# Kernel optimization log

Measured on AMD Instinct MI355X. Metric: run time of the kernel, lower is better.

Reference implementation:

```python
import jax, jax.numpy as jnp
import numpy as np

N_ATOMS = 8192
N_PAIRS = 65536
F = 128        # n_atombasis
R = 20         # n_radialbasis
B = 5          # graph_n_blocks
EPS = 1e-8     # stability constant


def setup_inputs() -> dict:
    key = jax.random.key(0)
    ks = jax.random.split(key, 16)
    rn = lambda k, shape, s=0.05: jax.random.normal(k, shape, dtype=jnp.float32) * s
    return {
        "features": jax.random.normal(ks[0], (N_ATOMS, F), jnp.float32),
        "distances": jax.random.uniform(ks[1], (N_PAIRS,), jnp.float32, 0.5, 5.0),
        "vectors": jax.random.normal(ks[2], (N_PAIRS, 3), jnp.float32),
        "cutoffs": jax.random.uniform(ks[3], (N_PAIRS,), jnp.float32),
        "rbfs": jax.random.normal(ks[4], (N_PAIRS, R), jnp.float32),
        "filter_W": rn(ks[5], (R, B * 3 * F)),
        "filter_b": jnp.zeros((B * 3 * F,), jnp.float32),
        "int_W1": rn(ks[6], (B, F, F)),
        "int_b1": jnp.zeros((B, F), jnp.float32),
        "int_W2": rn(ks[7], (B, F, 3 * F)),
        "int_b2": jnp.zeros((B, 3 * F), jnp.float32),
        "mix_Wv": rn(ks[8], (B, F, 2 * F)),
        "mix_W1": rn(ks[9], (B, 2 * F, F)),
        "mix_b1": jnp.zeros((B, F), jnp.float32),
        "mix_W2": rn(ks[10], (B, F, 3 * F)),
        "mix_b2": jnp.zeros((B, 3 * F), jnp.float32),
        "idx_i": jax.random.randint(ks[11], (N_PAIRS,), 0, N_ATOMS),
        "idx_j": jax.random.randint(ks[12], (N_PAIRS,), 0, N_ATOMS),
    }


def reference(features, distances, vectors, cutoffs, rbfs,
              filter_W, filter_b, int_W1, int_b1, int_W2, int_b2,
              mix_Wv, mix_W1, mix_b1, mix_W2, mix_b2, idx_i, idx_j):
    n_atoms = features.shape[0]
    # Cutoff-weighted radial filters, one (3F) chunk per block: [P, B*3F]
    descriptors = (rbfs @ filter_W + filter_b) * cutoffs[:, None]
    dir_ij = vectors / distances[:, None]                       # [P, 3]

    q = features[:, None, :]                                    # [N, 1, F]
    mu = jnp.zeros((n_atoms, 3, F), dtype=features.dtype)       # [N, 3, F]

    for b in range(B):
        # --- interaction block ---
        x = jax.nn.silu(q @ int_W1[b] + int_b1[b]) @ int_W2[b] + int_b2[b]  # [N,1,3F]
        Wij = descriptors[:, None, b * 3 * F:(b + 1) * 3 * F]               # [P,1,3F]
        xj = x[idx_j] * Wij                                                 # [P,1,3F]
        muj = mu[idx_j]                                                     # [P,3,F]
        dq, dmuR, dmumu = jnp.split(xj, 3, axis=-1)                         # [P,1,F] each
        dmu = dmuR * dir_ij[:, :, None] + dmumu * muj                       # [P,3,F]
        q = q + jax.ops.segment_sum(dq, idx_i, num_segments=n_atoms)
        mu = mu + jax.ops.segment_sum(dmu, idx_i, num_segments=n_atoms)

        # --- mixing block ---
        mu_V, mu_W = jnp.split(mu @ mix_Wv[b], 2, axis=-1)                  # [N,3,F] each
        mu_Vn = jnp.sqrt(jnp.sum(mu_V ** 2, axis=-2, keepdims=True) + EPS)  # [N,1,F]
        ctx = jnp.concatenate([q, mu_Vn], axis=-1)                          # [N,1,2F]
        y = jax.nn.silu(ctx @ mix_W1[b] + mix_b1[b]) @ mix_W2[b] + mix_b2[b]
        dq_i, dmu_i, dqmu_i = jnp.split(y, 3, axis=-1)                      # [N,1,F] each
        q = q + dq_i + dqmu_i * jnp.sum(mu_V * mu_W, axis=1, keepdims=True)
        mu = mu + dmu_i * mu_W

    return q[:, 0, :], mu
```

## Files before the change

### kernel.cpp

```cpp
#include <hip/hip_runtime.h>
#include <hip/hip_bf16.h>

#define NA 8192
#define NP 65536
#define WROW 1920
#define CAP 40

typedef short short8 __attribute__((ext_vector_type(8)));
typedef short short4v __attribute__((ext_vector_type(4)));
typedef float floatx4 __attribute__((ext_vector_type(4)));

static __device__ __forceinline__ short f2bf(float f) {
    union { float f; unsigned u; } v; v.f = f;
    unsigned r = v.u + 0x7FFF + ((v.u >> 16) & 1);
    return (short)(r >> 16);
}
static __device__ __forceinline__ float bf2f(short s) {
    union { unsigned u; float f; } v;
    v.u = ((unsigned)(unsigned short)s) << 16;
    return v.f;
}
static __device__ __forceinline__ unsigned char f2fp8(float f) {
    int p = __builtin_amdgcn_cvt_pk_fp8_f32(f, 0.f, 0, false);
    return (unsigned char)(p & 0xFF);
}
static __device__ __forceinline__ float fp82f(unsigned char b) {
    return __builtin_amdgcn_cvt_f32_fp8((int)b, 0);
}
static __device__ __forceinline__ float silu(float v) {
    return v / (1.f + __expf(-v));
}

static __device__ __forceinline__ void swz(const float* __restrict__ src,
                                           short* __restrict__ dst,
                                           int K, int N, int idx) {
    int kn = K * N;
    int b = idx / kn;
    int r = idx - b * kn;
    int tile = r >> 9, li = r & 511;
    int lane = li >> 3, bb = li & 7;
    int Kt = K >> 5;
    int nt = tile / Kt, kt = tile - nt * Kt;
    int k = kt * 32 + (lane >> 4) * 8 + bb;
    int n = nt * 16 + (lane & 15);
    dst[idx] = f2bf(src[b * kn + k * N + n]);
}

__global__ __launch_bounds__(256) void k_setup(const float* __restrict__ iW1,
                                               const float* __restrict__ iW2,
                                               const float* __restrict__ mWv,
                                               const float* __restrict__ mW1,
                                               const float* __restrict__ mW2,
                                               const float* __restrict__ fW,
                                               short* __restrict__ W1t,
                                               short* __restrict__ W2t,
                                               short* __restrict__ Wvt,
                                               short* __restrict__ mW1t,
                                               short* __restrict__ mW2t,
                                               short* __restrict__ fWt,
                                               const float* __restrict__ feat,
                                               float* __restrict__ q,
                                               float* __restrict__ mu,
                                               short* __restrict__ q_bf,
                                               unsigned* __restrict__ xarr0,
                                               unsigned* __restrict__ muarr0,
                                               int* __restrict__ cursor) {
    int idx = blockIdx.x * 256 + threadIdx.x;
    if (idx < 962560) {
        if (idx < 81920)       { swz(iW1, W1t, 128, 128, idx); return; }
        idx -= 81920;
        if (idx < 245760)      { swz(iW2, W2t, 128, 384, idx); return; }
        idx -= 245760;
        if (idx < 163840)      { swz(mWv, Wvt, 128, 256, idx); return; }
        idx -= 163840;
        if (idx < 163840)      { swz(mW1, mW1t, 256, 128, idx); return; }
        idx -= 163840;
        if (idx < 245760)      { swz(mW2, mW2t, 128, 384, idx); return; }
        idx -= 245760;
        {
            int b = idx / 12288;
            int r = idx - b * 12288;
            int nt = r >> 9;
            int li = r & 511;
            int lane = li >> 3, bb = li & 7;
            int k = (lane >> 4) * 8 + bb;
            int n = nt * 16 + (lane & 15);
            fWt[b * 12288 + r] = (k < 20) ? f2bf(fW[k * WROW + b * 384 + n]) : (short)0;
        }
        return;
    }
    idx -= 962560;
    if (idx < NA * 128) { float v = feat[idx]; q[idx] = v; q_bf[idx] = f2bf(v); xarr0[idx] = 0u; }
    if (idx < NA * 256) muarr0[idx] = 0u;
    mu[idx] = 0.f;
    if (idx < NA) cursor[idx] = 0;
}

__global__ __launch_bounds__(256) void k_fillprep(const int* __restrict__ idx_i,
                                                  const int* __restrict__ idx_j,
                                                  int* __restrict__ cursor,
                                                  const float* __restrict__ cut,
                                                  const float* __restrict__ dist,
                                                  const float* __restrict__ vec,
                                                  const float* __restrict__ rbfs,
                                                  float* __restrict__ cut_csr,
                                                  float4* __restrict__ dirj,
                                                  short* __restrict__ rbf_c) {
    int p = blockIdx.x * 256 + threadIdx.x;
    if (p >= NP) return;
    int i = idx_i[p];
    int pos = atomicAdd(&cursor[i], 1);
    if (pos >= CAP) return;
    int e = i * CAP + pos;
    float c = cut[p];
    cut_csr[e] = c;
    float invd = 1.f / dist[p];
    float4 d;
    d.x = vec[p * 3 + 0] * invd;
    d.y = vec[p * 3 + 1] * invd;
    d.z = vec[p * 3 + 2] * invd;
    d.w = __int_as_float(idx_j[p]);
    dirj[e] = d;
    #pragma unroll
    for (int k = 0; k < 20; ++k) rbf_c[e * 32 + k] = f2bf(rbfs[p * 20 + k] * c);
    #pragma unroll
    for (int k = 20; k < 32; ++k) rbf_c[e * 32 + k] = 0;
}

__global__ __launch_bounds__(256) void k_x(const short* __restrict__ q_bf,
                                           const short* __restrict__ W1sw,
                                           const short* __restrict__ W2sw,
                                           const float* __restrict__ b1,
                                           const float* __restrict__ b2,
                                           unsigned char* __restrict__ xarr) {
    __shared__ __align__(16) short qtile[16 * 136];
    __shared__ __align__(16) short hs[16 * 136];
    int t = threadIdx.x;
    int wv = t >> 6, lane = t & 63, quad = lane >> 4, l16 = lane & 15;
    int a0 = blockIdx.x * 16;

    #pragma unroll
    for (int it = 0; it < 2; ++it) {
        int c = it * 256 + t;
        int row = c >> 5, col4 = c & 31;
        *(short4v*)(qtile + row * 136 + col4 * 4) =
            *(const short4v*)(q_bf + (a0 + row) * 128 + col4 * 4);
    }
    __syncthreads();

    floatx4 acc0 = {0.f, 0.f, 0.f, 0.f}, acc1 = {0.f, 0.f, 0.f, 0.f};
    #pragma unroll
    for (int kk = 0; kk < 4; ++kk) {
        short8 a  = *(const short8*)(qtile + l16 * 136 + kk * 32 + quad * 8);
        short8 b0 = *(const short8*)(W1sw + ((wv * 2 + 0) * 4 + kk) * 512 + lane * 8);
        short8 bq = *(const short8*)(W1sw + ((wv * 2 + 1) * 4 + kk) * 512 + lane * 8);
        acc0 = __builtin_amdgcn_mfma_f32_16x16x32_bf16(a, b0, acc0, 0, 0, 0);
        acc1 = __builtin_amdgcn_mfma_f32_16x16x32_bf16(a, bq, acc1, 0, 0, 0);
    }
    __syncthreads();
    {
        int n0 = wv * 32 + l16;
        float bia0 = b1[n0], bia1 = b1[n0 + 16];
        #pragma unroll
        for (int r = 0; r < 4; ++r) {
            int m = quad * 4 + r;
            hs[m * 136 + n0]      = f2bf(silu(acc0[r] + bia0));
            hs[m * 136 + n0 + 16] = f2bf(silu(acc1[r] + bia1));
        }
    }
    __syncthreads();
    floatx4 acc[6];
    #pragma unroll
    for (int jj = 0; jj < 6; ++jj) acc[jj] = {0.f, 0.f, 0.f, 0.f};
    #pragma unroll
    for (int kk = 0; kk < 4; ++kk) {
        short8 a = *(const short8*)(hs + l16 * 136 + kk * 32 + quad * 8);
        #pragma unroll
        for (int jj = 0; jj < 6; ++jj) {
            short8 b = *(const short8*)(W2sw + ((wv * 6 + jj) * 4 + kk) * 512 + lane * 8);
            acc[jj] = __builtin_amdgcn_mfma_f32_16x16x32_bf16(a, b, acc[jj], 0, 0, 0);
        }
    }
    #pragma unroll
    for (int jj = 0; jj < 6; ++jj) {
        int n = wv * 96 + jj * 16 + l16;
        float bia = b2[n];
        #pragma unroll
        for (int r = 0; r < 4; ++r) {
            int m = quad * 4 + r;
            xarr[(size_t)((a0 + m) * 128 + (n & 127)) * 4 + (n >> 7)] =
                f2fp8(acc[jj][r] + bia);
        }
    }
}

__global__ __launch_bounds__(256, 4) void k_gather(const unsigned* __restrict__ xarr_r,
                                                   const uint2* __restrict__ muarr_r,
                                                   const short* __restrict__ rbf_c,
                                                   const short* __restrict__ fWt,
                                                   const float* __restrict__ fbp,
                                                   const float4* __restrict__ dirj,
                                                   const float* __restrict__ cut_csr,
                                                   const int* __restrict__ cursor,
                                                   short* __restrict__ dqg,
                                                   short* __restrict__ dmug) {
    __shared__ short dlds[16 * 392];
    __shared__ float pm[3 * 512];
    int i = blockIdx.x;
    int t = threadIdx.x;
    int wv = t >> 6, lane = t & 63, quad = lane >> 4, l16 = lane & 15;
    int start = i * CAP;

    float4 dj[4];
    #pragma unroll
    for (int m = 0; m < 4; ++m) dj[m] = dirj[start + wv + 4 * m];
    short8 afrag = *(const short8*)(rbf_c + (size_t)(start + l16) * 32 + quad * 8);
    float cc[4];
    #pragma unroll
    for (int r = 0; r < 4; ++r) cc[r] = cut_csr[start + quad * 4 + r];

    int cnt = cursor[i];
    if (cnt > CAP) cnt = CAP;
    int end = start + cnt;

    float acc[8];
    #pragma unroll
    for (int k = 0; k < 8; ++k) acc[k] = 0.f;

    for (int e0 = start; e0 < end; e0 += 16) {
        if (e0 > start) {
            __syncthreads();
            #pragma unroll
            for (int m = 0; m < 4; ++m) dj[m] = dirj[e0 + wv + 4 * m];
            afrag = *(const short8*)(rbf_c + (size_t)(e0 + l16) * 32 + quad * 8);
            #pragma unroll
            for (int r = 0; r < 4; ++r) cc[r] = cut_csr[e0 + quad * 4 + r];
        }
        int clen = end - e0; if (clen > 16) clen = 16;
        #pragma unroll
        for (int nt = 0; nt < 6; ++nt) {
            int col = wv * 96 + nt * 16 + l16;
            short8 bfr = *(const short8*)(fWt + (wv * 6 + nt) * 512 + lane * 8);
            floatx4 z = {0.f, 0.f, 0.f, 0.f};
            floatx4 ad = __builtin_amdgcn_mfma_f32_16x16x32_bf16(afrag, bfr, z, 0, 0, 0);
            float fbv = fbp[col];
            dlds[(quad * 4 + 0) * 392 + col] = f2bf(ad[0] + fbv * cc[0]);
            dlds[(quad * 4 + 1) * 392 + col] = f2bf(ad[1] + fbv * cc[1]);
            dlds[(quad * 4 + 2) * 392 + col] = f2bf(ad[2] + fbv * cc[2]);
            dlds[(quad * 4 + 3) * 392 + col] = f2bf(ad[3] + fbv * cc[3]);
        }
        unsigned xl[4], xh[4]; uint2 ml[4], mh[4];
        #pragma unroll
        for (int m = 0; m < 4; ++m) {
            int le = wv + 4 * m;
            int j = (le < clen) ? __float_as_int(dj[m].w) : 0;
            const unsigned* xb_ = xarr_r + (size_t)j * 128 + lane;
            xl[m] = xb_[0];
            xh[m] = xb_[64];
            const uint2* mb_ = muarr_r + (size_t)j * 128 + lane;
            ml[m] = mb_[0];
            mh[m] = mb_[64];
        }
        __syncthreads();
        #pragma unroll
        for (int m = 0; m < 4; ++m) {
            int le = wv + 4 * m;
            if (le < clen) {
                float wa0 = bf2f(dlds[le * 392 + lane]);
                float wb0 = bf2f(dlds[le * 392 + 128 + lane]);
                float wc0 = bf2f(dlds[le * 392 + 256 + lane]);
                float wa1 = bf2f(dlds[le * 392 + 64 + lane]);
                float wb1 = bf2f(dlds[le * 392 + 192 + lane]);
                float wc1 = bf2f(dlds[le * 392 + 320 + lane]);
                {
                    float x0 = fp82f((unsigned char)(xl[m] & 0xFF));
                    float x1 = fp82f((unsigned char)((xl[m] >> 8) & 0xFF));
                    float x2 = fp82f((unsigned char)((xl[m] >> 16) & 0xFF));
                    float u0 = bf2f((short)(ml[m].x & 0xFFFF));
                    float u1 = bf2f((short)(ml[m].x >> 16));
                    float u2 = bf2f((short)(ml[m].y & 0xFFFF));
                    acc[0] += x0 * wa0;
                    float xb = x1 * wb0, xc = x2 * wc0;
                    acc[1] += xb * dj[m].x + xc * u0;
                    acc[2] += xb * dj[m].y + xc * u1;
                    acc[3] += xb * dj[m].z + xc * u2;
                }
                {
                    float x0 = fp82f((unsigned char)(xh[m] & 0xFF));
                    float x1 = fp82f((unsigned char)((xh[m] >> 8) & 0xFF));
                    float x2 = fp82f((unsigned char)((xh[m] >> 16) & 0xFF));
                    float u0 = bf2f((short)(mh[m].x & 0xFFFF));
                    float u1 = bf2f((short)(mh[m].x >> 16));
                    float u2 = bf2f((short)(mh[m].y & 0xFFFF));
                    acc[4] += x0 * wa1;
                    float xb = x1 * wb1, xc = x2 * wc1;
                    acc[5] += xb * dj[m].x + xc * u0;
                    acc[6] += xb * dj[m].y + xc * u1;
                    acc[7] += xb * dj[m].z + xc * u2;
                }
            }
        }
    }
    if (wv) {
        float* p = pm + (wv - 1) * 512;
        #pragma unroll
        for (int arr = 0; arr < 4; ++arr) {
            p[arr * 128 + lane]      = acc[arr];
            p[arr * 128 + 64 + lane] = acc[arr + 4];
        }
    }
    __syncthreads();
    if (wv == 0) {
        #pragma unroll
        for (int hi = 0; hi < 2; ++hi) {
            int f = lane + hi * 64;
            float s[4];
            #pragma unroll
            for (int arr = 0; arr < 4; ++arr)
                s[arr] = acc[arr + 4 * hi]
                       + pm[0 * 512 + arr * 128 + f]
                       + pm[1 * 512 + arr * 128 + f]
                       + pm[2 * 512 + arr * 128 + f];
            dqg[i * 128 + f]            = f2bf(s[0]);
            dmug[(i * 3 + 0) * 128 + f] = f2bf(s[1]);
            dmug[(i * 3 + 1) * 128 + f] = f2bf(s[2]);
            dmug[(i * 3 + 2) * 128 + f] = f2bf(s[3]);
        }
    }
}

__global__ __launch_bounds__(512, 4) void k_mixx(const float* __restrict__ mu_ro,
                                                 const short* __restrict__ dmug,
                                                 const float* __restrict__ q_ro,
                                                 const short* __restrict__ dqg,
                                                 const short* __restrict__ Wvsw,
                                                 const short* __restrict__ W1sw,
                                                 const short* __restrict__ W2sw,
                                                 const float* __restrict__ b1,
                                                 const float* __restrict__ b2,
                                                 float* __restrict__ q,
                                                 float* __restrict__ mu,
                                                 unsigned* __restrict__ xarr_w,
                                                 uint2* __restrict__ muarr_w,
                                                 const short* __restrict__ xW1sw,
                                                 const short* __restrict__ xW2sw,
                                                 const float* __restrict__ xb1,
                                                 const float* __restrict__ xb2,
                                                 int do_x) {
    __shared__ __align__(16) char smem[51968];
    short* ms    = (short*)(smem);
    short* qtile = (short*)(smem + 13056);
    short* Vv    = (short*)(smem + 17408);
    short* hs    = (short*)(smem + 17408);
    short* Vw    = (short*)(smem + 30464);
    short* vnb   = (short*)(smem + 43520);
    short* sb    = (short*)(smem + 47872);
    unsigned char* xls = (unsigned char*)(smem + 43520);
    int t = threadIdx.x;
    int wv = t >> 6, lane = t & 63, quad = lane >> 4, l16 = lane & 15;
    int a0 = blockIdx.x * 16;
    int co = wv * 16 + l16;

    float qnf[4];
    float mnf[4][3];
    #pragma unroll
    for (int r = 0; r < 4; ++r) {
        int m = quad * 4 + r;
        int ga = a0 + m;
        int gq = ga * 128 + co;
        qnf[r] = q_ro[gq] + bf2f(dqg[gq]);
        qtile[m * 136 + co] = f2bf(qnf[r]);
        #pragma unroll
        for (int d = 0; d < 3; ++d) {
            int gm = (ga * 3 + d) * 128 + co;
            mnf[r][d] = mu_ro[gm] + bf2f(dmug[gm]);
            ms[(m * 3 + d) * 136 + co] = f2bf(mnf[r][d]);
        }
    }
    __syncthreads();

    {
        floatx4 acc[3][2];
        #pragma unroll
        for (int mt = 0; mt < 3; ++mt)
            #pragma unroll
            for (int nt = 0; nt < 2; ++nt) acc[mt][nt] = {0.f, 0.f, 0.f, 0.f};
        #pragma unroll
        for (int kk = 0; kk < 4; ++kk) {
            short8 a[3];
            #pragma unroll
            for (int mt = 0; mt < 3; ++mt)
                a[mt] = *(const short8*)(ms + (mt * 16 + l16) * 136 + kk * 32 + quad * 8);
            #pragma unroll
            for (int nt = 0; nt < 2; ++nt) {
                short8 b = *(const short8*)(Wvsw + ((wv * 2 + nt) * 4 + kk) * 512 + lane * 8);
                #pragma unroll
                for (int mt = 0; mt < 3; ++mt)
                    acc[mt][nt] = __builtin_amdgcn_mfma_f32_16x16x32_bf16(a[mt], b, acc[mt][nt], 0, 0, 0);
            }
        }
        #pragma unroll
        for (int mt = 0; mt < 3; ++mt)
            #pragma unroll
            for (int nt = 0; nt < 2; ++nt)
                #pragma unroll
                for (int r = 0; r < 4; ++r) {
                    int row = mt * 16 + quad * 4 + r;
                    int col = wv * 32 + nt * 16 + l16;
                    short v = f2bf(acc[mt][nt][r]);
                    if (col < 128) Vv[row * 136 + col] = v;
                    else           Vw[row * 136 + col - 128] = v;
                }
    }
    __syncthreads();
    #pragma unroll
    for (int k = 0; k < 4; ++k) {
        int idx = k * 512 + t;
        int a = idx >> 7, c = idx & 127;
        float v0 = bf2f(Vv[(a * 3 + 0) * 136 + c]);
        float v1 = bf2f(Vv[(a * 3 + 1) * 136 + c]);
        float v2 = bf2f(Vv[(a * 3 + 2) * 136 + c]);
        float w0 = bf2f(Vw[(a * 3 + 0) * 136 + c]);
        float w1 = bf2f(Vw[(a * 3 + 1) * 136 + c]);
        float w2 = bf2f(Vw[(a * 3 + 2) * 136 + c]);
        vnb[a * 136 + c] = f2bf(sqrtf(v0 * v0 + v1 * v1 + v2 * v2 + 1e-8f));
        sb[a * 128 + c]  = f2bf(v0 * w0 + v1 * w1 + v2 * w2);
    }
    __syncthreads();
    {
        floatx4 acc0 = {0.f, 0.f, 0.f, 0.f};
        #pragma unroll
        for (int kk = 0; kk < 8; ++kk) {
            short8 a;
            if (kk < 4)
                a = *(const short8*)(qtile + l16 * 136 + kk * 32 + quad * 8);
            else
                a = *(const short8*)(vnb + l16 * 136 + (kk - 4) * 32 + quad * 8);
            short8 b0 = *(const short8*)(W1sw + (wv * 8 + kk) * 512 + lane * 8);
            acc0 = __builtin_amdgcn_mfma_f32_16x16x32_bf16(a, b0, acc0, 0, 0, 0);
        }
        int n0 = wv * 16 + l16;
        float bia0 = b1[n0];
        #pragma unroll
        for (int r = 0; r < 4; ++r) {
            int m = quad * 4 + r;
            hs[m * 136 + n0] = f2bf(silu(acc0[r] + bia0));
        }
    }
    __syncthreads();
    {
        floatx4 accB[3];
        #pragma unroll
        for (int c = 0; c < 3; ++c) accB[c] = {0.f, 0.f, 0.f, 0.f};
        #pragma unroll
        for (int kk = 0; kk < 4; ++kk) {
            short8 a = *(const short8*)(hs + l16 * 136 + kk * 32 + quad * 8);
            #pragma unroll
            for (int c = 0; c < 3; ++c) {
                short8 b = *(const short8*)(W2sw + ((c * 8 + wv) * 4 + kk) * 512 + lane * 8);
                accB[c] = __builtin_amdgcn_mfma_f32_16x16x32_bf16(a, b, accB[c], 0, 0, 0);
            }
        }
        float bq_  = b2[co];
        float bm_  = b2[128 + co];
        float bqm_ = b2[256 + co];
        #pragma unroll
        for (int r = 0; r < 4; ++r) {
            int m = quad * 4 + r;
            int ga = a0 + m;
            float dq   = accB[0][r] + bq_;
            float dmu  = accB[1][r] + bm_;
            float dqmu = accB[2][r] + bqm_;
            float sv = bf2f(sb[m * 128 + co]);
            int gq = ga * 128 + co;
            float qn = qnf[r] + dq + dqmu * sv;
            q[gq] = qn;
            qtile[m * 136 + co] = f2bf(qn);
            float mn[3];
            #pragma unroll
            for (int d = 0; d < 3; ++d) {
                int gm = (ga * 3 + d) * 128 + co;
                float mw = bf2f(Vw[(m * 3 + d) * 136 + co]);
                mn[d] = mnf[r][d] + dmu * mw;
                mu[gm] = mn[d];
            }
            if (do_x) {
                uint2 mw2;
                mw2.x = (unsigned)(unsigned short)f2bf(mn[0]) |
                        ((unsigned)(unsigned short)f2bf(mn[1]) << 16);
                mw2.y = (unsigned)(unsigned short)f2bf(mn[2]);
                muarr_w[gq] = mw2;
            }
        }
    }
    if (!do_x) return;
    __syncthreads();
    {
        floatx4 acc0 = {0.f, 0.f, 0.f, 0.f};
        #pragma unroll
        for (int kk = 0; kk < 4; ++kk) {
            short8 a  = *(const short8*)(qtile + l16 * 136 + kk * 32 + quad * 8);
            short8 b0 = *(const short8*)(xW1sw + (wv * 4 + kk) * 512 + lane * 8);
            acc0 = __builtin_amdgcn_mfma_f32_16x16x32_bf16(a, b0, acc0, 0, 0, 0);
        }
        int n0 = wv * 16 + l16;
        float bia0 = xb1[n0];
        #pragma unroll
        for (int r = 0; r < 4; ++r) {
            int m = quad * 4 + r;
            hs[m * 136 + n0] = f2bf(silu(acc0[r] + bia0));
        }
    }
    __syncthreads();
    {
        floatx4 acc[3];
        #pragma unroll
        for (int jj = 0; jj < 3; ++jj) acc[jj] = {0.f, 0.f, 0.f, 0.f};
        #pragma unroll
        for (int kk = 0; kk < 4; ++kk) {
            short8 a = *(const short8*)(hs + l16 * 136 + kk * 32 + quad * 8);
            #pragma unroll
            for (int jj = 0; jj < 3; ++jj) {
                short8 b = *(const short8*)(xW2sw + ((wv * 3 + jj) * 4 + kk) * 512 + lane * 8);
                acc[jj] = __builtin_amdgcn_mfma_f32_16x16x32_bf16(a, b, acc[jj], 0, 0, 0);
            }
        }
        #pragma unroll
        for (int jj = 0; jj < 3; ++jj) {
            int n = wv * 48 + jj * 16 + l16;
            float bia = xb2[n];
            #pragma unroll
            for (int r = 0; r < 4; ++r) {
                int m = quad * 4 + r;
                xls[(m * 128 + (n & 127)) * 4 + (n >> 7)] = f2fp8(acc[jj][r] + bia);
            }
        }
    }
    __syncthreads();
    {
        const unsigned* xlsu = (const unsigned*)xls;
        unsigned* xw = xarr_w + (size_t)a0 * 128;
        #pragma unroll
        for (int k = 0; k < 4; ++k) {
            int idx = k * 512 + t;
            xw[idx] = xlsu[idx];
        }
    }
}

extern "C" void kernel_launch(void* const* d_in, const int* in_sizes, int n_in,
                              void* d_out, int out_size, void* d_ws, size_t ws_size,
                              hipStream_t stream) {
    const float* feat = (const float*)d_in[0];
    const float* dist = (const float*)d_in[1];
    const float* vec  = (const float*)d_in[2];
    const float* cut  = (const float*)d_in[3];
    const float* rbfs = (const float*)d_in[4];
    const float* fW   = (const float*)d_in[5];
    const float* fb   = (const float*)d_in[6];
    const float* iW1  = (const float*)d_in[7];
    const float* ib1  = (const float*)d_in[8];
    const float* iW2  = (const float*)d_in[9];
    const float* ib2  = (const float*)d_in[10];
    const float* mWv  = (const float*)d_in[11];
    const float* mW1  = (const float*)d_in[12];
    const float* mb1  = (const float*)d_in[13];
    const float* mW2  = (const float*)d_in[14];
    const float* mb2  = (const float*)d_in[15];
    const int* idx_i  = (const int*)d_in[16];
    const int* idx_j  = (const int*)d_in[17];

    float* q  = (float*)d_out;
    float* mu = (float*)d_out + NA * 128;

    char* w = (char*)d_ws;
    unsigned* xarr0  = (unsigned*)(w);
    unsigned* xarr1  = (unsigned*)(w + 4194304);
    uint2*    muarr0 = (uint2*)(w + 8388608);
    uint2*    muarr1 = (uint2*)(w + 16777216);
    short* dqg     = (short*)(w + 25165824);
    short* dmug    = (short*)(w + 27262976);
    short* q_bf    = (short*)(w + 33554432);
    short* W1t     = (short*)(w + 35651584);
    short* W2t     = (short*)(w + 35815424);
    short* Wvt     = (short*)(w + 36306944);
    short* mW1t    = (short*)(w + 36634624);
    short* mW2t    = (short*)(w + 36962304);
    short* fWt     = (short*)(w + 37453824);
    int*   cursor  = (int*)(w + 37576704);
    float4* dirj   = (float4*)(w + 37609472);
    float* cut_csr = (float*)(w + 42852608);
    short* rbf_c   = (short*)(w + 44163392);

    k_setup<<<16048, 256, 0, stream>>>(iW1, iW2, mWv, mW1, mW2, fW,
                                       W1t, W2t, Wvt, mW1t, mW2t, fWt,
                                       feat, q, mu, q_bf, xarr0, (unsigned*)muarr0, cursor);
    k_fillprep<<<NP / 256, 256, 0, stream>>>(idx_i, idx_j, cursor, cut, dist, vec,
                                             rbfs, cut_csr, dirj, rbf_c);

    k_x<<<NA / 16, 256, 0, stream>>>(q_bf, W1t, W2t, ib1, ib2, (unsigned char*)xarr0);
    unsigned* xa[2] = {xarr0, xarr1};
    uint2*    ma[2] = {muarr0, muarr1};
    for (int b = 0; b < 5; ++b) {
        int bn = (b + 1) % 5;
        k_gather<<<NA, 256, 0, stream>>>(xa[b & 1], ma[b & 1], rbf_c, fWt + b * 12288,
                                         fb + b * 384, dirj, cut_csr, cursor,
                                         dqg, dmug);
        k_mixx<<<NA / 16, 512, 0, stream>>>(mu, dmug, q, dqg,
                                            Wvt + b * 32768,
                                            mW1t + b * 32768, mW2t + b * 49152,
                                            mb1 + b * 128, mb2 + b * 384,
                                            q, mu,
                                            xa[(b + 1) & 1], ma[(b + 1) & 1],
                                            W1t + bn * 16384, W2t + bn * 49152,
                                            ib1 + bn * 128, ib2 + bn * 384,
                                            (b < 4) ? 1 : 0);
    }
}
```

Measured before the change: 368.9 us.

## Vectorize gather loads, split mixing MFMA chains, use memsets for zero-init

The gather kernel now has each lane own two adjacent features, so x, mu, descriptor and partial-sum accesses become wider vector loads and stores in place of pairs of strided scalar ones. The mixing MLP's first layer splits its single 8-step MFMA dependency chain into two independent 4-step chains that are summed afterwards, which exposes more instruction-level parallelism. Zero-initialisation of cursor, mu and muarr0 moves from the setup kernel to hipMemsetAsync calls, and xarr0 is no longer zeroed. This shrinks the setup grid but adds three extra stream operations and changes the lane-to-feature mapping.

```diff
diff --git a/kernel.cpp b/kernel.cpp
--- a/kernel.cpp
+++ b/kernel.cpp
@@ -60,11 +60,7 @@
                                                short* __restrict__ fWt,
                                                const float* __restrict__ feat,
                                                float* __restrict__ q,
-                                               float* __restrict__ mu,
-                                               short* __restrict__ q_bf,
-                                               unsigned* __restrict__ xarr0,
-                                               unsigned* __restrict__ muarr0,
-                                               int* __restrict__ cursor) {
+                                               short* __restrict__ q_bf) {
     int idx = blockIdx.x * 256 + threadIdx.x;
     if (idx < 962560) {
         if (idx < 81920)       { swz(iW1, W1t, 128, 128, idx); return; }
@@ -90,10 +86,7 @@
         return;
     }
     idx -= 962560;
-    if (idx < NA * 128) { float v = feat[idx]; q[idx] = v; q_bf[idx] = f2bf(v); xarr0[idx] = 0u; }
-    if (idx < NA * 256) muarr0[idx] = 0u;
-    mu[idx] = 0.f;
-    if (idx < NA) cursor[idx] = 0;
+    if (idx < NA * 128) { float v = feat[idx]; q[idx] = v; q_bf[idx] = f2bf(v); }
 }
 
 __global__ __launch_bounds__(256) void k_fillprep(const int* __restrict__ idx_i,
@@ -210,6 +203,7 @@
     int t = threadIdx.x;
     int wv = t >> 6, lane = t & 63, quad = lane >> 4, l16 = lane & 15;
     int start = i * CAP;
+    int f0 = lane * 2;
 
     float4 dj[4];
     #pragma unroll
@@ -249,36 +243,33 @@
             dlds[(quad * 4 + 2) * 392 + col] = f2bf(ad[2] + fbv * cc[2]);
             dlds[(quad * 4 + 3) * 392 + col] = f2bf(ad[3] + fbv * cc[3]);
         }
-        unsigned xl[4], xh[4]; uint2 ml[4], mh[4];
+        uint2 xr[4]; uint4 mr[4];
         #pragma unroll
         for (int m = 0; m < 4; ++m) {
             int le = wv + 4 * m;
             int j = (le < clen) ? __float_as_int(dj[m].w) : 0;
-            const unsigned* xb_ = xarr_r + (size_t)j * 128 + lane;
-            xl[m] = xb_[0];
-            xh[m] = xb_[64];
-            const uint2* mb_ = muarr_r + (size_t)j * 128 + lane;
-            ml[m] = mb_[0];
-            mh[m] = mb_[64];
+            xr[m] = *(const uint2*)(xarr_r + (size_t)j * 128 + f0);
+            mr[m] = *(const uint4*)(muarr_r + (size_t)j * 128 + f0);
         }
         __syncthreads();
         #pragma unroll
         for (int m = 0; m < 4; ++m) {
             int le = wv + 4 * m;
             if (le < clen) {
-                float wa0 = bf2f(dlds[le * 392 + lane]);
-                float wb0 = bf2f(dlds[le * 392 + 128 + lane]);
-                float wc0 = bf2f(dlds[le * 392 + 256 + lane]);
-                float wa1 = bf2f(dlds[le * 392 + 64 + lane]);
-                float wb1 = bf2f(dlds[le * 392 + 192 + lane]);
-                float wc1 = bf2f(dlds[le * 392 + 320 + lane]);
+                unsigned wa = *(const unsigned*)(dlds + le * 392 + f0);
+                unsigned wb = *(const unsigned*)(dlds + le * 392 + 128 + f0);
+                unsigned wc = *(const unsigned*)(dlds + le * 392 + 256 + f0);
+                float wa0 = bf2f((short)(wa & 0xFFFF)), wa1 = bf2f((short)(wa >> 16));
+                float wb0 = bf2f((short)(wb & 0xFFFF)), wb1 = bf2f((short)(wb >> 16));
+                float wc0 = bf2f((short)(wc & 0xFFFF)), wc1 = bf2f((short)(wc >> 16));
                 {
-                    float x0 = fp82f((unsigned char)(xl[m] & 0xFF));
-                    float x1 = fp82f((unsigned char)((xl[m] >> 8) & 0xFF));
-                    float x2 = fp82f((unsigned char)((xl[m] >> 16) & 0xFF));
-                    float u0 = bf2f((short)(ml[m].x & 0xFFFF));
-                    float u1 = bf2f((short)(ml[m].x >> 16));
-                    float u2 = bf2f((short)(ml[m].y & 0xFFFF));
+                    unsigned xw = xr[m].x;
+                    float x0 = fp82f((unsigned char)(xw & 0xFF));
+                    float x1 = fp82f((unsigned char)((xw >> 8) & 0xFF));
+                    float x2 = fp82f((unsigned char)((xw >> 16) & 0xFF));
+                    float u0 = bf2f((short)(mr[m].x & 0xFFFF));
+                    float u1 = bf2f((short)(mr[m].x >> 16));
+                    float u2 = bf2f((short)(mr[m].y & 0xFFFF));
                     acc[0] += x0 * wa0;
                     float xb = x1 * wb0, xc = x2 * wc0;
                     acc[1] += xb * dj[m].x + xc * u0;
@@ -286,12 +277,13 @@
                     acc[3] += xb * dj[m].z + xc * u2;
                 }
                 {
-                    float x0 = fp82f((unsigned char)(xh[m] & 0xFF));
-                    float x1 = fp82f((unsigned char)((xh[m] >> 8) & 0xFF));
-                    float x2 = fp82f((unsigned char)((xh[m] >> 16) & 0xFF));
-                    float u0 = bf2f((short)(mh[m].x & 0xFFFF));
-                    float u1 = bf2f((short)(mh[m].x >> 16));
-                    float u2 = bf2f((short)(mh[m].y & 0xFFFF));
+                    unsigned xw = xr[m].y;
+                    float x0 = fp82f((unsigned char)(xw & 0xFF));
+                    float x1 = fp82f((unsigned char)((xw >> 8) & 0xFF));
+                    float x2 = fp82f((unsigned char)((xw >> 16) & 0xFF));
+                    float u0 = bf2f((short)(mr[m].z & 0xFFFF));
+                    float u1 = bf2f((short)(mr[m].z >> 16));
+                    float u2 = bf2f((short)(mr[m].w & 0xFFFF));
                     acc[4] += x0 * wa1;
                     float xb = x1 * wb1, xc = x2 * wc1;
                     acc[5] += xb * dj[m].x + xc * u0;
@@ -305,26 +297,23 @@
         float* p = pm + (wv - 1) * 512;
         #pragma unroll
         for (int arr = 0; arr < 4; ++arr) {
-            p[arr * 128 + lane]      = acc[arr];
-            p[arr * 128 + 64 + lane] = acc[arr + 4];
+            float2 v; v.x = acc[arr]; v.y = acc[arr + 4];
+            *(float2*)(p + arr * 128 + f0) = v;
         }
     }
     __syncthreads();
     if (wv == 0) {
         #pragma unroll
-        for (int hi = 0; hi < 2; ++hi) {
-            int f = lane + hi * 64;
-            float s[4];
-            #pragma unroll
-            for (int arr = 0; arr < 4; ++arr)
-                s[arr] = acc[arr + 4 * hi]
-                       + pm[0 * 512 + arr * 128 + f]
-                       + pm[1 * 512 + arr * 128 + f]
-                       + pm[2 * 512 + arr * 128 + f];
-            dqg[i * 128 + f]            = f2bf(s[0]);
-            dmug[(i * 3 + 0) * 128 + f] = f2bf(s[1]);
-            dmug[(i * 3 + 1) * 128 + f] = f2bf(s[2]);
-            dmug[(i * 3 + 2) * 128 + f] = f2bf(s[3]);
+        for (int arr = 0; arr < 4; ++arr) {
+            float2 p0 = *(const float2*)(pm + 0 * 512 + arr * 128 + f0);
+            float2 p1 = *(const float2*)(pm + 1 * 512 + arr * 128 + f0);
+            float2 p2 = *(const float2*)(pm + 2 * 512 + arr * 128 + f0);
+            float sl = acc[arr]     + p0.x + p1.x + p2.x;
+            float sh = acc[arr + 4] + p0.y + p1.y + p2.y;
+            unsigned o = (unsigned)(unsigned short)f2bf(sl) |
+                         ((unsigned)(unsigned short)f2bf(sh) << 16);
+            if (arr == 0) *(unsigned*)(dqg + i * 128 + f0) = o;
+            else          *(unsigned*)(dmug + (i * 3 + arr - 1) * 128 + f0) = o;
         }
     }
 }
@@ -428,23 +417,23 @@
     }
     __syncthreads();
     {
-        floatx4 acc0 = {0.f, 0.f, 0.f, 0.f};
-        #pragma unroll
-        for (int kk = 0; kk < 8; ++kk) {
-            short8 a;
-            if (kk < 4)
-                a = *(const short8*)(qtile + l16 * 136 + kk * 32 + quad * 8);
-            else
-                a = *(const short8*)(vnb + l16 * 136 + (kk - 4) * 32 + quad * 8);
-            short8 b0 = *(const short8*)(W1sw + (wv * 8 + kk) * 512 + lane * 8);
-            acc0 = __builtin_amdgcn_mfma_f32_16x16x32_bf16(a, b0, acc0, 0, 0, 0);
+        floatx4 accq = {0.f, 0.f, 0.f, 0.f};
+        floatx4 accv = {0.f, 0.f, 0.f, 0.f};
+        #pragma unroll
+        for (int kk = 0; kk < 4; ++kk) {
+            short8 aq = *(const short8*)(qtile + l16 * 136 + kk * 32 + quad * 8);
+            short8 av = *(const short8*)(vnb + l16 * 136 + kk * 32 + quad * 8);
+            short8 bq = *(const short8*)(W1sw + (wv * 8 + kk) * 512 + lane * 8);
+            short8 bv = *(const short8*)(W1sw + (wv * 8 + 4 + kk) * 512 + lane * 8);
+            accq = __builtin_amdgcn_mfma_f32_16x16x32_bf16(aq, bq, accq, 0, 0, 0);
+            accv = __builtin_amdgcn_mfma_f32_16x16x32_bf16(av, bv, accv, 0, 0, 0);
         }
         int n0 = wv * 16 + l16;
         float bia0 = b1[n0];
         #pragma unroll
         for (int r = 0; r < 4; ++r) {
             int m = quad * 4 + r;
-            hs[m * 136 + n0] = f2bf(silu(acc0[r] + bia0));
+            hs[m * 136 + n0] = f2bf(silu(accq[r] + accv[r] + bia0));
         }
     }
     __syncthreads();
@@ -592,9 +581,13 @@
     float* cut_csr = (float*)(w + 42852608);
     short* rbf_c   = (short*)(w + 44163392);
 
-    k_setup<<<16048, 256, 0, stream>>>(iW1, iW2, mWv, mW1, mW2, fW,
-                                       W1t, W2t, Wvt, mW1t, mW2t, fWt,
-                                       feat, q, mu, q_bf, xarr0, (unsigned*)muarr0, cursor);
+    hipMemsetAsync(cursor, 0, NA * 4, stream);
+    hipMemsetAsync(muarr0, 0, NA * 128 * 8, stream);
+    hipMemsetAsync(mu, 0, (size_t)NA * 384 * 4, stream);
+
+    k_setup<<<7856, 256, 0, stream>>>(iW1, iW2, mWv, mW1, mW2, fW,
+                                      W1t, W2t, Wvt, mW1t, mW2t, fWt,
+                                      feat, q, q_bf);
     k_fillprep<<<NP / 256, 256, 0, stream>>>(idx_i, idx_j, cursor, cut, dist, vec,
                                              rbfs, cut_csr, dirj, rbf_c);
 
```

Result: slower. 398.5 us (+8.0%).
